# Kernel optimization log

Measured on AMD Instinct MI355X. Metric: run time of the kernel, lower is better.

Reference implementation:

```python
import jax, jax.numpy as jnp
import numpy as np

N_NODES = 100000
N_EDGES = 3200000
D_IN = 256
D_OUT = 256


def setup_inputs() -> dict:
    key = jax.random.key(0)
    k1, k2, k3, k4, k5 = jax.random.split(key, 5)
    features = jax.random.normal(k1, (N_NODES, D_IN), dtype=jnp.float32)
    # xavier_uniform init for the weight
    limit = np.sqrt(6.0 / (D_IN + D_OUT)).astype(np.float32)
    weight = jax.random.uniform(k2, (D_IN, D_OUT), minval=-limit, maxval=limit, dtype=jnp.float32)
    adj_row = jax.random.randint(k3, (N_EDGES,), 0, N_NODES, dtype=jnp.int64)
    adj_col = jax.random.randint(k4, (N_EDGES,), 0, N_NODES, dtype=jnp.int64)
    adj_val = jax.random.uniform(k5, (N_EDGES,), dtype=jnp.float32)
    return {"features": features, "weight": weight, "adj_row": adj_row,
            "adj_col": adj_col, "adj_val": adj_val}


def reference(features, weight, adj_row, adj_col, adj_val):
    # support = features @ W   (dense GEMM)
    support = features @ weight                      # [N, D_OUT]
    # spmm: out[i] = sum_e val[e] * support[col[e]] for edges with row[e] == i
    gathered = adj_val[:, None] * support[adj_col]   # [E, D_OUT]
    out = jax.ops.segment_sum(gathered, adj_row, num_segments=features.shape[0])
    return jax.nn.relu(out)
```

## Files before the change

### kernel.cpp

```cpp
#include <hip/hip_runtime.h>
#include <hip/hip_bf16.h>

#define N_NODES 100000
#define N_EDGES 3200000
#define NBUCK   391
#define NBLKE   782
#define CAP_R   9600

typedef short v8s __attribute__((ext_vector_type(8)));
typedef float v4f __attribute__((ext_vector_type(4)));
typedef unsigned short v8u __attribute__((ext_vector_type(8)));

__device__ __forceinline__ unsigned short f2b(float x) {
    __hip_bfloat16 h = __float2bfloat16(x);
    return *reinterpret_cast<unsigned short*>(&h);
}
__device__ __forceinline__ float b2f(unsigned short u) {
    return __uint_as_float(((unsigned int)u) << 16);
}

__device__ __forceinline__ void gld16(const void* g, void* l) {
    __builtin_amdgcn_global_load_lds(
        (const __attribute__((address_space(1))) void*)g,
        (__attribute__((address_space(3))) void*)l, 16, 0, 0);
}

__global__ void transpose_b(const float* __restrict__ B, unsigned short* __restrict__ BT) {
    int n = blockIdx.x;
    int k = threadIdx.x;
    BT[n * 256 + k] = f2b(B[k * 256 + n]);
}

__global__ __launch_bounds__(512)
void gemm_dma(const float* __restrict__ A, const unsigned short* __restrict__ BT,
              unsigned short* __restrict__ C) {
    __shared__ __align__(16) float          sA[128 * 64];
    __shared__ __align__(16) unsigned short sB[256 * 64];

    const int tid  = threadIdx.x;
    const int wave = tid >> 6;
    const int lane = tid & 63;
    const int quad = lane >> 4;
    const int l16  = lane & 15;
    const int row0 = blockIdx.x * 128;

    v4f acc[16];
#pragma unroll
    for (int t = 0; t < 16; t++) acc[t] = (v4f){0.f, 0.f, 0.f, 0.f};

    const int ml = wave * 16 + l16;

    for (int ks = 0; ks < 4; ks++) {
        const int kbase = ks * 64;
#pragma unroll
        for (int i = 0; i < 4; i++) {
            int s = i * 512 + tid;
            int m = s >> 4;
            int c = (s & 15) ^ (m & 15);
            int row = row0 + m;
            if (row >= N_NODES) row = row0;
            gld16(A + (size_t)row * 256 + kbase + c * 4, (char*)sA + (size_t)s * 16);
        }
#pragma unroll
        for (int i = 0; i < 4; i++) {
            int s = i * 512 + tid;
            int n = s >> 3;
            int c = (s & 7) ^ (n & 7);
            gld16(BT + (size_t)n * 256 + kbase + c * 8, (char*)sB + (size_t)s * 16);
        }
        __syncthreads();

#pragma unroll
        for (int sub = 0; sub < 2; sub++) {
            int ca  = sub * 8 + 2 * quad;
            int pa0 = ml * 16 + (ca ^ (ml & 15));
            int pa1 = ml * 16 + ((ca + 1) ^ (ml & 15));
            v4f lo = *(const v4f*)&sA[pa0 * 4];
            v4f hi = *(const v4f*)&sA[pa1 * 4];
            v8s af;
            af[0] = (short)f2b(lo[0]); af[1] = (short)f2b(lo[1]);
            af[2] = (short)f2b(lo[2]); af[3] = (short)f2b(lo[3]);
            af[4] = (short)f2b(hi[0]); af[5] = (short)f2b(hi[1]);
            af[6] = (short)f2b(hi[2]); af[7] = (short)f2b(hi[3]);
            int cb = sub * 4 + quad;
#pragma unroll
            for (int t = 0; t < 16; t++) {
                int n  = t * 16 + l16;
                int pb = n * 8 + (cb ^ (n & 7));
                v8s bf = *(const v8s*)&sB[pb * 8];
                acc[t] = __builtin_amdgcn_mfma_f32_16x16x32_bf16(af, bf, acc[t], 0, 0, 0);
            }
        }
        __syncthreads();
    }

    const int grow_base = row0 + wave * 16 + quad * 4;
#pragma unroll
    for (int t = 0; t < 16; t++) {
#pragma unroll
        for (int r = 0; r < 4; r++) {
            int grow = grow_base + r;
            if (grow < N_NODES)
                C[(size_t)grow * 256 + t * 16 + l16] = f2b(acc[t][r]);
        }
    }
}

__global__ __launch_bounds__(512)
void bin4_kernel(const int* __restrict__ row, const int* __restrict__ col,
                 const float* __restrict__ val,
                 unsigned int* __restrict__ bucketK, unsigned short* __restrict__ bucketV,
                 unsigned int* __restrict__ runs) {
    __shared__ int cnt[512];
    __shared__ int lcur[512];
    __shared__ int wsum[8];
    __shared__ __align__(16) unsigned int   skey[4096];
    __shared__ unsigned short sval[4096];

    const int tid = threadIdx.x;
    const int e0  = blockIdx.x * 4096;

    int r[8], c[8];
    unsigned short v[8];
#pragma unroll
    for (int j = 0; j < 8; j++) {
        int e = e0 + j * 512 + tid;
        if (e < N_EDGES) {
            r[j] = row[e]; c[j] = col[e];
            v[j] = (unsigned short)((((unsigned int)__float_as_int(val[e]) + 0x8000u) >> 16) & 0x7FFFu);
        } else r[j] = -1;
    }

    cnt[tid] = 0;
    __syncthreads();
#pragma unroll
    for (int j = 0; j < 8; j++)
        if (r[j] >= 0) atomicAdd(&cnt[r[j] >> 8], 1);
    __syncthreads();

    const int lane = tid & 63, w = tid >> 6;
    int x = cnt[tid];
    int inc = x;
#pragma unroll
    for (int d = 1; d < 64; d <<= 1) {
        int t = __shfl_up(inc, d);
        if (lane >= d) inc += t;
    }
    if (lane == 63) wsum[w] = inc;
    __syncthreads();
    int pre = 0;
#pragma unroll
    for (int k = 0; k < 8; k++) pre += (k < w) ? wsum[k] : 0;
    int excl = pre + inc - x;
    lcur[tid] = excl;
    if (tid < NBUCK)
        runs[(size_t)tid * NBLKE + blockIdx.x] =
            ((unsigned int)excl << 13) | (unsigned int)x;
    __syncthreads();

#pragma unroll
    for (int j = 0; j < 8; j++) {
        if (r[j] >= 0) {
            int b = r[j] >> 8;
            int q = atomicAdd(&lcur[b], 1);
            skey[q] = ((unsigned int)(r[j] & 255) << 17) | (unsigned int)c[j];
            sval[q] = v[j];
        }
    }
    __syncthreads();

    int tot = N_EDGES - e0;
    if (tot > 4096) tot = 4096;
    for (int i = tid; i < tot; i += 512) {
        bucketK[e0 + i] = skey[i];
        bucketV[e0 + i] = sval[i];
    }
}

__global__ __launch_bounds__(1024)
void csort4_kernel(const unsigned int* __restrict__ bucketK,
                   const unsigned short* __restrict__ bucketV,
                   const unsigned int* __restrict__ runs,
                   unsigned int* __restrict__ csr,
                   int* __restrict__ offs, int* __restrict__ counts) {
    __shared__ unsigned int   skey[CAP_R];
    __shared__ unsigned short sval[CAP_R];
    __shared__ int rstart[NBLKE];
    __shared__ int rofs[NBLKE];
    __shared__ int rcnt[NBLKE];
    __shared__ int h[256];
    __shared__ int cur[256];
    __shared__ int wsum4[4];
    __shared__ int stot;

    const int tid  = threadIdx.x;
    const int b    = blockIdx.x;
    const int base = b * CAP_R;
    const int w    = tid >> 6, lane = tid & 63;

    if (tid == 0) stot = 0;
    if (tid < 256) h[tid] = 0;
    __syncthreads();

    if (tid < NBLKE) {
        unsigned int d = runs[(size_t)b * NBLKE + tid];
        int c = (int)(d & 0x1FFFu);
        rstart[tid] = tid * 4096 + (int)(d >> 13);
        rcnt[tid]   = c;
        rofs[tid]   = c ? atomicAdd(&stot, c) : 0;
    }
    __syncthreads();

    for (int rr = w; rr < NBLKE; rr += 16) {
        int c   = rcnt[rr];
        int src = rstart[rr];
        int dst = rofs[rr];
        for (int i = lane; i < c; i += 64) {
            skey[dst + i] = bucketK[src + i];
            sval[dst + i] = bucketV[src + i];
        }
    }
    __syncthreads();

    const int n = stot;
    for (int i = tid; i < n; i += 1024)
        atomicAdd(&h[skey[i] >> 17], 1);
    __syncthreads();

    int x = 0, inc = 0;
    if (tid < 256) {
        x = h[tid];
        inc = x;
#pragma unroll
        for (int d = 1; d < 64; d <<= 1) {
            int t = __shfl_up(inc, d);
            if (lane >= d) inc += t;
        }
        if (lane == 63) wsum4[w] = inc;
    }
    __syncthreads();
    if (tid < 256) {
        int pre = 0;
#pragma unroll
        for (int k = 0; k < 4; k++) pre += (k < w) ? wsum4[k] : 0;
        int excl = pre + inc - x;
        int grow = b * 256 + tid;
        if (grow < N_NODES) {
            offs[grow]   = base + excl;
            counts[grow] = x;
        }
        cur[tid] = base + excl;
    }
    __syncthreads();

    for (int i = tid; i < n; i += 1024) {
        unsigned int k = skey[i];
        int rl = (int)(k >> 17);
        int p  = atomicAdd(&cur[rl], 1);
        csr[p] = ((unsigned int)sval[i] << 17) | (k & 0x1FFFFu);
    }
}

__global__ __launch_bounds__(256)
void spmm_half(const unsigned short* __restrict__ sup,
               const int* __restrict__ offs, const int* __restrict__ counts,
               const unsigned int* __restrict__ csr, float* __restrict__ out,
               const int cbase) {
    const int wave = threadIdx.x >> 6;
    const int lane = threadIdx.x & 63;
    const int row  = blockIdx.x * 4 + wave;
    if (row >= N_NODES) return;

    const int q   = lane >> 4;
    const int c16 = lane & 15;
    const unsigned short* supc = sup + cbase + c16 * 8;

    const int start = offs[row];
    const int deg   = counts[row];

    float a[8];
#pragma unroll
    for (int k = 0; k < 8; k++) a[k] = 0.f;

    for (int base2 = 0; base2 < deg; base2 += 64) {
        int nb = deg - base2;
        if (nb > 64) nb = 64;
        int c = 0;
        float v = 0.f;
        if (lane < nb) {
            unsigned int w = csr[start + base2 + lane];
            c = (int)(w & 0x1FFFFu);
            v = __uint_as_float((w >> 17) << 16);
        }
        int ng = (nb + 3) >> 2;
        int g = 0;
        for (; g + 4 <= ng; g += 4) {
            int cc[4]; float vv[4];
#pragma unroll
            for (int u = 0; u < 4; u++) {
                int idx = (g + u) * 4 + q;
                cc[u] = __shfl(c, idx);
                vv[u] = __shfl(v, idx);
            }
            v8u h[4];
#pragma unroll
            for (int u = 0; u < 4; u++)
                h[u] = *(const v8u*)(supc + (size_t)cc[u] * 256);
#pragma unroll
            for (int u = 0; u < 4; u++) {
#pragma unroll
                for (int k = 0; k < 8; k++)
                    a[k] += vv[u] * b2f(h[u][k]);
            }
        }
        for (; g < ng; g++) {
            int idx = g * 4 + q;
            int   cc = __shfl(c, idx);
            float vv = __shfl(v, idx);
            v8u h = *(const v8u*)(supc + (size_t)cc * 256);
#pragma unroll
            for (int k = 0; k < 8; k++)
                a[k] += vv * b2f(h[k]);
        }
    }

#pragma unroll
    for (int k = 0; k < 8; k++) {
        a[k] += __shfl_xor(a[k], 16);
        a[k] += __shfl_xor(a[k], 32);
    }

    if (lane < 32) {
        int q2 = lane >> 4;
        int cl = lane & 15;
        float4 o;
        o.x = a[q2 * 4 + 0] > 0.f ? a[q2 * 4 + 0] : 0.f;
        o.y = a[q2 * 4 + 1] > 0.f ? a[q2 * 4 + 1] : 0.f;
        o.z = a[q2 * 4 + 2] > 0.f ? a[q2 * 4 + 2] : 0.f;
        o.w = a[q2 * 4 + 3] > 0.f ? a[q2 * 4 + 3] : 0.f;
        *(float4*)(out + (size_t)row * 256 + cbase + cl * 8 + q2 * 4) = o;
    }
}

extern "C" void kernel_launch(void* const* d_in, const int* in_sizes, int n_in,
                              void* d_out, int out_size, void* d_ws, size_t ws_size,
                              hipStream_t stream) {
    const float* features = (const float*)d_in[0];
    const float* weight   = (const float*)d_in[1];
    const int*   adj_row  = (const int*)d_in[2];
    const int*   adj_col  = (const int*)d_in[3];
    const float* adj_val  = (const float*)d_in[4];
    float* out = (float*)d_out;

    char* ws = (char*)d_ws;
    size_t off = 0;
    auto alloc = [&](size_t bytes) -> char* {
        char* p = ws + off;
        off = (off + bytes + 255) & ~(size_t)255;
        return p;
    };
    unsigned short* sup     = (unsigned short*)alloc((size_t)N_NODES * 256 * 2);
    unsigned short* BT      = (unsigned short*)alloc(256 * 256 * 2);
    int*            counts  = (int*)alloc((size_t)N_NODES * 4);
    int*            offsets = (int*)alloc((size_t)N_NODES * 4);
    unsigned int*   bucketK = (unsigned int*)alloc((size_t)N_EDGES * 4);
    unsigned short* bucketV = (unsigned short*)alloc((size_t)N_EDGES * 2);
    unsigned int*   runs    = (unsigned int*)alloc((size_t)NBUCK * NBLKE * 4);
    unsigned int*   csr     = (unsigned int*)alloc((size_t)NBUCK * CAP_R * 4);

    transpose_b<<<256, 256, 0, stream>>>(weight, BT);
    gemm_dma<<<782, 512, 0, stream>>>(features, BT, sup);
    bin4_kernel<<<NBLKE, 512, 0, stream>>>(adj_row, adj_col, adj_val, bucketK, bucketV, runs);
    csort4_kernel<<<NBUCK, 1024, 0, stream>>>(bucketK, bucketV, runs, csr, offsets, counts);
    spmm_half<<<25000, 256, 0, stream>>>(sup, offsets, counts, csr, out, 0);
    spmm_half<<<25000, 256, 0, stream>>>(sup, offsets, counts, csr, out, 128);
}
```

Measured before the change: 477.3 us.

## Reuse atomic ranks in binning, scan-based gather in csort, four-slice SpMM

The binning kernel now keeps the rank returned by the counting atomic and uses it to place each edge, so the second atomic pass is gone. The column-sort kernel replaces its atomic run-offset allocation and per-wave copy with a block-wide prefix scan plus a per-element binary search for the gather. It also reuses the histogram atomic ranks for the scatter. The SpMM is merged into one launch that splits the 256 columns into four 64-column slices, with 8 edges in flight per wave instead of 4, aiming for more memory-level parallelism and fewer launches. The binary search adds work per element, the tail loops now carry 10 rank registers, and each edge's csr entry is read by four slices instead of two.

```diff
diff --git a/kernel.cpp b/kernel.cpp
--- a/kernel.cpp
+++ b/kernel.cpp
@@ -107,12 +107,12 @@
 }
 
 __global__ __launch_bounds__(512)
-void bin4_kernel(const int* __restrict__ row, const int* __restrict__ col,
+void bin5_kernel(const int* __restrict__ row, const int* __restrict__ col,
                  const float* __restrict__ val,
                  unsigned int* __restrict__ bucketK, unsigned short* __restrict__ bucketV,
                  unsigned int* __restrict__ runs) {
     __shared__ int cnt[512];
-    __shared__ int lcur[512];
+    __shared__ int ls[512];
     __shared__ int wsum[8];
     __shared__ __align__(16) unsigned int   skey[4096];
     __shared__ unsigned short sval[4096];
@@ -120,7 +120,7 @@
     const int tid = threadIdx.x;
     const int e0  = blockIdx.x * 4096;
 
-    int r[8], c[8];
+    int r[8], c[8], rank[8];
     unsigned short v[8];
 #pragma unroll
     for (int j = 0; j < 8; j++) {
@@ -135,7 +135,7 @@
     __syncthreads();
 #pragma unroll
     for (int j = 0; j < 8; j++)
-        if (r[j] >= 0) atomicAdd(&cnt[r[j] >> 8], 1);
+        if (r[j] >= 0) rank[j] = atomicAdd(&cnt[r[j] >> 8], 1);
     __syncthreads();
 
     const int lane = tid & 63, w = tid >> 6;
@@ -152,7 +152,7 @@
 #pragma unroll
     for (int k = 0; k < 8; k++) pre += (k < w) ? wsum[k] : 0;
     int excl = pre + inc - x;
-    lcur[tid] = excl;
+    ls[tid] = excl;
     if (tid < NBUCK)
         runs[(size_t)tid * NBLKE + blockIdx.x] =
             ((unsigned int)excl << 13) | (unsigned int)x;
@@ -162,7 +162,7 @@
     for (int j = 0; j < 8; j++) {
         if (r[j] >= 0) {
             int b = r[j] >> 8;
-            int q = atomicAdd(&lcur[b], 1);
+            int q = ls[b] + rank[j];
             skey[q] = ((unsigned int)(r[j] & 255) << 17) | (unsigned int)c[j];
             sval[q] = v[j];
         }
@@ -178,7 +178,7 @@
 }
 
 __global__ __launch_bounds__(1024)
-void csort4_kernel(const unsigned int* __restrict__ bucketK,
+void csort5_kernel(const unsigned int* __restrict__ bucketK,
                    const unsigned short* __restrict__ bucketV,
                    const unsigned int* __restrict__ runs,
                    unsigned int* __restrict__ csr,
@@ -186,94 +186,113 @@
     __shared__ unsigned int   skey[CAP_R];
     __shared__ unsigned short sval[CAP_R];
     __shared__ int rstart[NBLKE];
-    __shared__ int rofs[NBLKE];
-    __shared__ int rcnt[NBLKE];
+    __shared__ int rofs[NBLKE + 1];
     __shared__ int h[256];
-    __shared__ int cur[256];
+    __shared__ int sbase[256];
+    __shared__ int wsum[16];
     __shared__ int wsum4[4];
-    __shared__ int stot;
 
     const int tid  = threadIdx.x;
     const int b    = blockIdx.x;
     const int base = b * CAP_R;
     const int w    = tid >> 6, lane = tid & 63;
 
-    if (tid == 0) stot = 0;
     if (tid < 256) h[tid] = 0;
-    __syncthreads();
-
+
+    int x = 0;
     if (tid < NBLKE) {
         unsigned int d = runs[(size_t)b * NBLKE + tid];
-        int c = (int)(d & 0x1FFFu);
+        x = (int)(d & 0x1FFFu);
         rstart[tid] = tid * 4096 + (int)(d >> 13);
-        rcnt[tid]   = c;
-        rofs[tid]   = c ? atomicAdd(&stot, c) : 0;
-    }
-    __syncthreads();
-
-    for (int rr = w; rr < NBLKE; rr += 16) {
-        int c   = rcnt[rr];
-        int src = rstart[rr];
-        int dst = rofs[rr];
-        for (int i = lane; i < c; i += 64) {
-            skey[dst + i] = bucketK[src + i];
-            sval[dst + i] = bucketV[src + i];
-        }
-    }
-    __syncthreads();
-
-    const int n = stot;
-    for (int i = tid; i < n; i += 1024)
-        atomicAdd(&h[skey[i] >> 17], 1);
-    __syncthreads();
-
-    int x = 0, inc = 0;
+    }
+    int inc = x;
+#pragma unroll
+    for (int d = 1; d < 64; d <<= 1) {
+        int t = __shfl_up(inc, d);
+        if (lane >= d) inc += t;
+    }
+    if (lane == 63) wsum[w] = inc;
+    __syncthreads();
+    int pre = 0;
+#pragma unroll
+    for (int k = 0; k < 16; k++) pre += (k < w) ? wsum[k] : 0;
+    int excl = pre + inc - x;
+    if (tid <= NBLKE) rofs[tid] = excl;
+    __syncthreads();
+
+    const int n = rofs[NBLKE];
+
+    for (int i = tid; i < n; i += 1024) {
+        int lo = 0, hi = NBLKE - 1;
+        while (lo < hi) {
+            int mid = (lo + hi + 1) >> 1;
+            if (rofs[mid] <= i) lo = mid; else hi = mid - 1;
+        }
+        int src = rstart[lo] + (i - rofs[lo]);
+        skey[i] = bucketK[src];
+        sval[i] = bucketV[src];
+    }
+    __syncthreads();
+
+    int rk[10];
+#pragma unroll
+    for (int k = 0; k < 10; k++) {
+        int i = tid + k * 1024;
+        if (i < n) rk[k] = atomicAdd(&h[skey[i] >> 17], 1);
+    }
+    __syncthreads();
+
+    int xx = 0, inc2 = 0;
     if (tid < 256) {
-        x = h[tid];
-        inc = x;
+        xx = h[tid];
+        inc2 = xx;
 #pragma unroll
         for (int d = 1; d < 64; d <<= 1) {
-            int t = __shfl_up(inc, d);
-            if (lane >= d) inc += t;
-        }
-        if (lane == 63) wsum4[w] = inc;
+            int t = __shfl_up(inc2, d);
+            if (lane >= d) inc2 += t;
+        }
+        if (lane == 63) wsum4[w] = inc2;
     }
     __syncthreads();
     if (tid < 256) {
-        int pre = 0;
-#pragma unroll
-        for (int k = 0; k < 4; k++) pre += (k < w) ? wsum4[k] : 0;
-        int excl = pre + inc - x;
+        int pre4 = 0;
+#pragma unroll
+        for (int k = 0; k < 4; k++) pre4 += (k < w) ? wsum4[k] : 0;
+        int e2 = pre4 + inc2 - xx;
         int grow = b * 256 + tid;
         if (grow < N_NODES) {
-            offs[grow]   = base + excl;
-            counts[grow] = x;
-        }
-        cur[tid] = base + excl;
-    }
-    __syncthreads();
-
-    for (int i = tid; i < n; i += 1024) {
-        unsigned int k = skey[i];
-        int rl = (int)(k >> 17);
-        int p  = atomicAdd(&cur[rl], 1);
-        csr[p] = ((unsigned int)sval[i] << 17) | (k & 0x1FFFFu);
+            offs[grow]   = base + e2;
+            counts[grow] = xx;
+        }
+        sbase[tid] = base + e2;
+    }
+    __syncthreads();
+
+#pragma unroll
+    for (int k = 0; k < 10; k++) {
+        int i = tid + k * 1024;
+        if (i < n) {
+            unsigned int kk = skey[i];
+            int rl = (int)(kk >> 17);
+            csr[sbase[rl] + rk[k]] = ((unsigned int)sval[i] << 17) | (kk & 0x1FFFFu);
+        }
     }
 }
 
 __global__ __launch_bounds__(256)
-void spmm_half(const unsigned short* __restrict__ sup,
-               const int* __restrict__ offs, const int* __restrict__ counts,
-               const unsigned int* __restrict__ csr, float* __restrict__ out,
-               const int cbase) {
+void spmm_s4(const unsigned short* __restrict__ sup,
+             const int* __restrict__ offs, const int* __restrict__ counts,
+             const unsigned int* __restrict__ csr, float* __restrict__ out) {
+    const int slice  = blockIdx.x & 3;
+    const int rowblk = blockIdx.x >> 2;
     const int wave = threadIdx.x >> 6;
     const int lane = threadIdx.x & 63;
-    const int row  = blockIdx.x * 4 + wave;
+    const int row  = rowblk * 4 + wave;
     if (row >= N_NODES) return;
 
-    const int q   = lane >> 4;
-    const int c16 = lane & 15;
-    const unsigned short* supc = sup + cbase + c16 * 8;
+    const int q  = lane >> 3;
+    const int c8 = lane & 7;
+    const unsigned short* supc = sup + slice * 64 + c8 * 8;
 
     const int start = offs[row];
     const int deg   = counts[row];
@@ -285,60 +304,47 @@
     for (int base2 = 0; base2 < deg; base2 += 64) {
         int nb = deg - base2;
         if (nb > 64) nb = 64;
-        int c = 0;
-        float v = 0.f;
-        if (lane < nb) {
-            unsigned int w = csr[start + base2 + lane];
-            c = (int)(w & 0x1FFFFu);
-            v = __uint_as_float((w >> 17) << 16);
-        }
-        int ng = (nb + 3) >> 2;
+        unsigned int wd = 0;
+        if (lane < nb) wd = csr[start + base2 + lane];
+        int ng = (nb + 7) >> 3;
         int g = 0;
-        for (; g + 4 <= ng; g += 4) {
-            int cc[4]; float vv[4];
-#pragma unroll
-            for (int u = 0; u < 4; u++) {
-                int idx = (g + u) * 4 + q;
-                cc[u] = __shfl(c, idx);
-                vv[u] = __shfl(v, idx);
-            }
-            v8u h[4];
-#pragma unroll
-            for (int u = 0; u < 4; u++)
-                h[u] = *(const v8u*)(supc + (size_t)cc[u] * 256);
-#pragma unroll
-            for (int u = 0; u < 4; u++) {
-#pragma unroll
-                for (int k = 0; k < 8; k++)
-                    a[k] += vv[u] * b2f(h[u][k]);
-            }
+        for (; g + 2 <= ng; g += 2) {
+            unsigned int w0 = __shfl(wd, g * 8 + q);
+            unsigned int w1 = __shfl(wd, g * 8 + 8 + q);
+            float v0 = __uint_as_float((w0 >> 17) << 16);
+            float v1 = __uint_as_float((w1 >> 17) << 16);
+            v8u h0 = *(const v8u*)(supc + (size_t)(w0 & 0x1FFFFu) * 256);
+            v8u h1 = *(const v8u*)(supc + (size_t)(w1 & 0x1FFFFu) * 256);
+#pragma unroll
+            for (int k = 0; k < 8; k++) a[k] += v0 * b2f(h0[k]);
+#pragma unroll
+            for (int k = 0; k < 8; k++) a[k] += v1 * b2f(h1[k]);
         }
         for (; g < ng; g++) {
-            int idx = g * 4 + q;
-            int   cc = __shfl(c, idx);
-            float vv = __shfl(v, idx);
-            v8u h = *(const v8u*)(supc + (size_t)cc * 256);
-#pragma unroll
-            for (int k = 0; k < 8; k++)
-                a[k] += vv * b2f(h[k]);
+            unsigned int w0 = __shfl(wd, g * 8 + q);
+            float v0 = __uint_as_float((w0 >> 17) << 16);
+            v8u h0 = *(const v8u*)(supc + (size_t)(w0 & 0x1FFFFu) * 256);
+#pragma unroll
+            for (int k = 0; k < 8; k++) a[k] += v0 * b2f(h0[k]);
         }
     }
 
 #pragma unroll
     for (int k = 0; k < 8; k++) {
+        a[k] += __shfl_xor(a[k], 8);
         a[k] += __shfl_xor(a[k], 16);
         a[k] += __shfl_xor(a[k], 32);
     }
 
-    if (lane < 32) {
-        int q2 = lane >> 4;
-        int cl = lane & 15;
-        float4 o;
-        o.x = a[q2 * 4 + 0] > 0.f ? a[q2 * 4 + 0] : 0.f;
-        o.y = a[q2 * 4 + 1] > 0.f ? a[q2 * 4 + 1] : 0.f;
-        o.z = a[q2 * 4 + 2] > 0.f ? a[q2 * 4 + 2] : 0.f;
-        o.w = a[q2 * 4 + 3] > 0.f ? a[q2 * 4 + 3] : 0.f;
-        *(float4*)(out + (size_t)row * 256 + cbase + cl * 8 + q2 * 4) = o;
+    if (lane < 8) {
+        float* op = out + (size_t)row * 256 + slice * 64 + lane * 8;
+        float4 o0, o1;
+        o0.x = fmaxf(a[0], 0.f); o0.y = fmaxf(a[1], 0.f);
+        o0.z = fmaxf(a[2], 0.f); o0.w = fmaxf(a[3], 0.f);
+        o1.x = fmaxf(a[4], 0.f); o1.y = fmaxf(a[5], 0.f);
+        o1.z = fmaxf(a[6], 0.f); o1.w = fmaxf(a[7], 0.f);
+        *(float4*)op       = o0;
+        *(float4*)(op + 4) = o1;
     }
 }
 
@@ -370,8 +376,7 @@
 
     transpose_b<<<256, 256, 0, stream>>>(weight, BT);
     gemm_dma<<<782, 512, 0, stream>>>(features, BT, sup);
-    bin4_kernel<<<NBLKE, 512, 0, stream>>>(adj_row, adj_col, adj_val, bucketK, bucketV, runs);
-    csort4_kernel<<<NBUCK, 1024, 0, stream>>>(bucketK, bucketV, runs, csr, offsets, counts);
-    spmm_half<<<25000, 256, 0, stream>>>(sup, offsets, counts, csr, out, 0);
-    spmm_half<<<25000, 256, 0, stream>>>(sup, offsets, counts, csr, out, 128);
-}
+    bin5_kernel<<<NBLKE, 512, 0, stream>>>(adj_row, adj_col, adj_val, bucketK, bucketV, runs);
+    csort5_kernel<<<NBUCK, 1024, 0, stream>>>(bucketK, bucketV, runs, csr, offsets, counts);
+    spmm_s4<<<100000, 256, 0, stream>>>(sup, offsets, counts, csr, out);
+}
```

Result: faster. 443.3 us (-7.1%).
